# Optimization experiments

Measured on AMD Instinct MI355X. Metric: run time of the kernel, lower is better.

The kernel has to match this reference:

```python
import jax, jax.numpy as jnp
import numpy as np

N = 100_000
E = 1_000_000
F_IN = 128
F_OUT = 64
NHOP = 2


def _xavier(k, shape, gain=1.414):
    fan_in, fan_out = shape
    std = gain * np.sqrt(2.0 / (fan_in + fan_out))
    return (jax.random.normal(k, shape) * std).astype(jnp.float32)


def setup_inputs() -> dict:
    key = jax.random.key(0)
    ks = jax.random.split(key, 8)
    x = jax.random.normal(ks[0], (N, F_IN), jnp.float32)
    edge_index = jax.random.randint(ks[1], (2, E), 0, N)
    edge_attr = jax.random.uniform(ks[2], (E,), jnp.float32)
    W0 = _xavier(ks[3], (F_IN, F_OUT))
    W1 = _xavier(ks[4], (F_IN, F_OUT))
    b0 = jnp.zeros((F_OUT,), jnp.float32)
    b1 = jnp.zeros((F_OUT,), jnp.float32)
    fc0 = _xavier(ks[5], (F_OUT, 1))
    fc1 = _xavier(ks[6], (F_OUT, 1))
    bf0 = jnp.zeros((1,), jnp.float32)
    bf1 = jnp.zeros((1,), jnp.float32)
    return dict(x=x, edge_index=edge_index, edge_attr=edge_attr,
                W0=W0, b0=b0, W1=W1, b1=b1,
                fc0=fc0, bf0=bf0, fc1=fc1, bf1=bf1)


def _spmm(row, col, val, v, n):
    # (A v)[r] = sum over edges (r -> c) of val * v[c]
    return jax.ops.segment_sum(val[:, None] * v[col], row, num_segments=n)


def _adaptive_enc(y, fc, bf):
    # NodeAdaptiveEncoder (eval mode): relu(y) + sigmoid(y@fc+bf) * min(y, 0)
    g = jax.nn.sigmoid(y @ fc + bf)  # [N, 1]
    return jnp.where(y < 0, 0.0, y) + g * jnp.where(y > 0, 0.0, y)


def reference(x, edge_index, edge_attr, W0, b0, W1, b1, fc0, bf0, fc1, bf1):
    n = x.shape[0]
    row, col = edge_index[0], edge_index[1]
    ones = jnp.ones((n, 1), x.dtype)
    params = [(W0, b0, fc0, bf0), (W1, b1, fc1, bf1)]
    outs = []
    for hop in range(NHOP):
        W, b, fc, bf = params[hop]
        h = x @ W  # [N, F_OUT]
        # identity attention; row_uniform norm of A^(hop+1) factors as
        # (A^(hop+1) h) / (A^(hop+1) 1) -- exact since spspmm sums duplicates.
        agg, deg = h, ones
        for _ in range(hop + 1):
            agg = _spmm(row, col, edge_attr, agg, n)
            deg = _spmm(row, col, edge_attr, deg, n)
        safe_deg = jnp.where(deg > 0, deg, 1.0)
        y = jnp.where(deg > 0, agg / safe_deg, 0.0)  # NaN mask for empty rows
        y = y + b
        outs.append(_adaptive_enc(y, fc, bf))
    return jnp.concatenate(outs, axis=1)  # [N, NHOP * F_OUT]
```

## Files before the change

kernel.cpp:

```cpp
#include <hip/hip_runtime.h>

#define F_IN 128
#define F_ALL 128
#define F_HOP 64

#define RPB_BITS 7
#define RPB 128
#define KB_MAX 1024
#define NBLK_BIN 512
#define ECAP 2048

typedef unsigned int uint;
typedef unsigned short ushort;
typedef __attribute__((ext_vector_type(8))) short short8v;
typedef __attribute__((ext_vector_type(4))) float float4v;

__device__ __forceinline__ uint pack_bf16(float lo, float hi) {
    uint ul = __float_as_uint(lo), uh = __float_as_uint(hi);
    ul += 0x7FFFu + ((ul >> 16) & 1u);
    uh += 0x7FFFu + ((uh >> 16) & 1u);
    return (ul >> 16) | (uh & 0xFFFF0000u);
}
__device__ __forceinline__ float bf_lo(uint h) { return __uint_as_float(h << 16); }
__device__ __forceinline__ float bf_hi(uint h) { return __uint_as_float(h & 0xFFFF0000u); }

__global__ __launch_bounds__(256) void gemm_hist_kernel(
    const float* __restrict__ x, const float* __restrict__ W0,
    const float* __restrict__ W1, uint* __restrict__ H2,
    const int* __restrict__ ei, int* __restrict__ bhist,
    int N, int E, int K, int gemmBlocks) {
    __shared__ ushort Wlds[16384];

    if ((int)blockIdx.x >= gemmBlocks) {
        int* h = (int*)Wlds;
        const int hb = blockIdx.x - gemmBlocks;
        for (int i = threadIdx.x; i < K; i += 256) h[i] = 0;
        __syncthreads();
        const int chunk = (E + NBLK_BIN - 1) / NBLK_BIN;
        const int s = hb * chunk;
        const int e = min(s + chunk, E);
        for (int j = s + threadIdx.x; j < e; j += 256)
            atomicAdd(&h[__builtin_nontemporal_load(ei + j) >> RPB_BITS], 1);
        __syncthreads();
        for (int i = threadIdx.x; i < K; i += 256)
            bhist[hb * KB_MAX + i] = h[i];
        return;
    }

    {
        const int t = threadIdx.x;
        #pragma unroll
        for (int i = 0; i < 8; ++i) {
            const int e    = t + 256 * i;
            const int lane = e & 63;
            const int tile = e >> 6;
            const int kt   = tile >> 3;
            const int nt   = tile & 7;
            const int k0   = kt * 32 + (lane >> 4) * 8;
            const int n    = nt * 16 + (lane & 15);
            const float* src = (n < 64) ? (W0 + n) : (W1 + (n - 64));
            float v[8];
            #pragma unroll
            for (int j = 0; j < 8; ++j) v[j] = src[(size_t)(k0 + j) * F_HOP];
            uint4 o;
            o.x = pack_bf16(v[0], v[1]);
            o.y = pack_bf16(v[2], v[3]);
            o.z = pack_bf16(v[4], v[5]);
            o.w = pack_bf16(v[6], v[7]);
            *((uint4*)Wlds + e) = o;
        }
    }
    __syncthreads();

    const int wv   = threadIdx.x >> 6;
    const int lane = threadIdx.x & 63;
    const int rbase = blockIdx.x * 64 + wv * 16;
    if (rbase >= N) return;

    const int m    = lane & 15;
    const int quad = lane >> 4;
    const float* xrow = x + (size_t)(rbase + m) * F_IN + quad * 8;

    float4v acc[8];
    #pragma unroll
    for (int t = 0; t < 8; ++t) acc[t] = (float4v){0.f, 0.f, 0.f, 0.f};

    #pragma unroll
    for (int kt = 0; kt < 4; ++kt) {
        const float4v xa = __builtin_nontemporal_load((const float4v*)(xrow + kt * 32));
        const float4v xb = __builtin_nontemporal_load((const float4v*)(xrow + kt * 32 + 4));
        union { uint4 u; short8v s; } av;
        av.u.x = pack_bf16(xa[0], xa[1]);
        av.u.y = pack_bf16(xa[2], xa[3]);
        av.u.z = pack_bf16(xb[0], xb[1]);
        av.u.w = pack_bf16(xb[2], xb[3]);
        #pragma unroll
        for (int nt = 0; nt < 8; ++nt) {
            union { uint4 u; short8v s; } bv;
            bv.u = *((const uint4*)Wlds + (kt * 8 + nt) * 64 + lane);
            acc[nt] = __builtin_amdgcn_mfma_f32_16x16x32_bf16(av.s, bv.s, acc[nt], 0, 0, 0);
        }
    }

    #pragma unroll
    for (int t = 0; t < 4; ++t) {
        #pragma unroll
        for (int i = 0; i < 4; ++i) {
            const int r = rbase + quad * 4 + i;
            H2[(size_t)r * F_HOP + t * 16 + m] = pack_bf16(acc[t][i], acc[t + 4][i]);
        }
    }
}

__global__ __launch_bounds__(512) void blockscan_kernel(
    int* __restrict__ bhist, int* __restrict__ btot) {
    __shared__ int wsum[8];
    const int b = blockIdx.x;
    const int t = threadIdx.x;
    const int s = bhist[t * KB_MAX + b];
    int v = s;
    #pragma unroll
    for (int d = 1; d < 64; d <<= 1) {
        int u = __shfl_up(v, (unsigned)d, 64);
        if ((t & 63) >= d) v += u;
    }
    if ((t & 63) == 63) wsum[t >> 6] = v;
    __syncthreads();
    int off = 0;
    #pragma unroll
    for (int i = 0; i < 8; ++i) if (i < (t >> 6)) off += wsum[i];
    bhist[t * KB_MAX + b] = off + v - s;
    if (t == 511) btot[b] = off + v;
}

__global__ __launch_bounds__(256) void bin_kernel(
    const int* __restrict__ ei, const float* __restrict__ ea,
    const int* __restrict__ bloc, const int* __restrict__ btot,
    int* __restrict__ bbase_g, int2* __restrict__ gbuf, int E, int K) {
    __shared__ int bb[KB_MAX];
    __shared__ int cur[KB_MAX];
    __shared__ int wsum[4];
    const int t = threadIdx.x;
    const int i0 = 4 * t;
    const int c0 = (i0     < K) ? btot[i0]     : 0;
    const int c1 = (i0 + 1 < K) ? btot[i0 + 1] : 0;
    const int c2 = (i0 + 2 < K) ? btot[i0 + 2] : 0;
    const int c3 = (i0 + 3 < K) ? btot[i0 + 3] : 0;
    const int s = c0 + c1 + c2 + c3;
    int v = s;
    #pragma unroll
    for (int d = 1; d < 64; d <<= 1) {
        int u = __shfl_up(v, (unsigned)d, 64);
        if ((t & 63) >= d) v += u;
    }
    if ((t & 63) == 63) wsum[t >> 6] = v;
    __syncthreads();
    {
        int off = 0;
        #pragma unroll
        for (int i = 0; i < 4; ++i) if (i < (t >> 6)) off += wsum[i];
        const int excl = off + v - s;
        if (i0     < K) bb[i0]     = excl;
        if (i0 + 1 < K) bb[i0 + 1] = excl + c0;
        if (i0 + 2 < K) bb[i0 + 2] = excl + c0 + c1;
        if (i0 + 3 < K) bb[i0 + 3] = excl + c0 + c1 + c2;
    }
    __syncthreads();
    if (blockIdx.x == 0) {
        for (int i = t; i < K; i += 256) bbase_g[i] = bb[i];
        if (t == 0) bbase_g[K] = E;
    }
    for (int i = t; i < K; i += 256)
        cur[i] = bb[i] + bloc[blockIdx.x * KB_MAX + i];
    __syncthreads();
    const int chunk = (E + NBLK_BIN - 1) / NBLK_BIN;
    const int s0 = blockIdx.x * chunk;
    const int e0 = min(s0 + chunk, E);
    for (int j = s0 + t; j < e0; j += 256) {
        const int r = __builtin_nontemporal_load(ei + j);
        const int c = __builtin_nontemporal_load(ei + E + j);
        const int vv = __float_as_int(__builtin_nontemporal_load(ea + j));
        const int b = r >> RPB_BITS;
        const int gp = atomicAdd(&cur[b], 1);
        gbuf[gp] = make_int2(c | ((r & (RPB - 1)) << 17), vv);
    }
}

__global__ __launch_bounds__(512) void pass1_kernel(
    const int* __restrict__ bbase, const int2* __restrict__ gbuf,
    const uint* __restrict__ H2,
    const float* __restrict__ b0, const float* __restrict__ fc0,
    const float* __restrict__ bf0,
    float* __restrict__ out, ushort* __restrict__ T16,
    float* __restrict__ dg1, int N) {
    __shared__ int2 ebuf[ECAP];
    __shared__ int cnt[RPB];
    __shared__ int rp[RPB + 1];
    __shared__ int wsum2[2];
    const int t = threadIdx.x;
    const int b = blockIdx.x;
    const int bstart = bbase[b];
    const int m = bbase[b + 1] - bstart;
    const int mc = (m < ECAP) ? m : ECAP;
    const int row0 = b << RPB_BITS;

    if (t < RPB) cnt[t] = 0;
    __syncthreads();
    for (int j = t; j < mc; j += 512) {
        const int2 p = gbuf[bstart + j];
        ebuf[j] = p;
        atomicAdd(&cnt[(p.x >> 17) & (RPB - 1)], 1);
    }
    __syncthreads();
    int sv = 0, vv = 0;
    if (t < RPB) {
        sv = cnt[t];
        vv = sv;
        #pragma unroll
        for (int d = 1; d < 64; d <<= 1) {
            int u = __shfl_up(vv, (unsigned)d, 64);
            if ((t & 63) >= d) vv += u;
        }
        if ((t & 63) == 63) wsum2[t >> 6] = vv;
    }
    __syncthreads();
    if (t < RPB) rp[t] = ((t >= 64) ? wsum2[0] : 0) + vv - sv;
    if (t == 0) rp[RPB] = mc;
    __syncthreads();
    if (t < RPB) cnt[t] = rp[t];
    __syncthreads();
    int2 pr[4]; int pp[4]; bool pvld[4];
    #pragma unroll
    for (int k2 = 0; k2 < 4; ++k2) {
        const int j = t + 512 * k2;
        pvld[k2] = (j < mc);
        if (pvld[k2]) {
            pr[k2] = ebuf[j];
            pp[k2] = atomicAdd(&cnt[(pr[k2].x >> 17) & (RPB - 1)], 1);
        }
    }
    __syncthreads();
    #pragma unroll
    for (int k2 = 0; k2 < 4; ++k2)
        if (pvld[k2]) ebuf[pp[k2]] = pr[k2];
    __syncthreads();

    const int l  = t & 15;
    const int g  = t >> 4;
    const int f0 = l * 4;
    const uint* __restrict__ H2b = H2 + f0;

    for (int k = 0; k < 4; ++k) {
        const int lr = g * 4 + k;
        const int r = row0 + lr;
        if (r >= N) break;
        const int jb = rp[lr], je = rp[lr + 1];

        float s00 = 0.f, s01 = 0.f, s02 = 0.f, s03 = 0.f;
        float s10 = 0.f, s11 = 0.f, s12 = 0.f, s13 = 0.f;
        float d = 0.f;
        int j = jb;
        for (; j + 4 <= je; j += 4) {
            const int2 e0 = ebuf[j], e1 = ebuf[j + 1], e2 = ebuf[j + 2], e3 = ebuf[j + 3];
            const uint4 h0 = *(const uint4*)(H2b + (size_t)(e0.x & 0x1FFFF) * F_HOP);
            const uint4 h1 = *(const uint4*)(H2b + (size_t)(e1.x & 0x1FFFF) * F_HOP);
            const uint4 h2 = *(const uint4*)(H2b + (size_t)(e2.x & 0x1FFFF) * F_HOP);
            const uint4 h3 = *(const uint4*)(H2b + (size_t)(e3.x & 0x1FFFF) * F_HOP);
            const float v0 = __int_as_float(e0.y), v1 = __int_as_float(e1.y);
            const float v2 = __int_as_float(e2.y), v3 = __int_as_float(e3.y);
            d += (v0 + v1) + (v2 + v3);
            s00 = fmaf(v0, bf_lo(h0.x), s00); s10 = fmaf(v0, bf_hi(h0.x), s10);
            s01 = fmaf(v0, bf_lo(h0.y), s01); s11 = fmaf(v0, bf_hi(h0.y), s11);
            s02 = fmaf(v0, bf_lo(h0.z), s02); s12 = fmaf(v0, bf_hi(h0.z), s12);
            s03 = fmaf(v0, bf_lo(h0.w), s03); s13 = fmaf(v0, bf_hi(h0.w), s13);
            s00 = fmaf(v1, bf_lo(h1.x), s00); s10 = fmaf(v1, bf_hi(h1.x), s10);
            s01 = fmaf(v1, bf_lo(h1.y), s01); s11 = fmaf(v1, bf_hi(h1.y), s11);
            s02 = fmaf(v1, bf_lo(h1.z), s02); s12 = fmaf(v1, bf_hi(h1.z), s12);
            s03 = fmaf(v1, bf_lo(h1.w), s03); s13 = fmaf(v1, bf_hi(h1.w), s13);
            s00 = fmaf(v2, bf_lo(h2.x), s00); s10 = fmaf(v2, bf_hi(h2.x), s10);
            s01 = fmaf(v2, bf_lo(h2.y), s01); s11 = fmaf(v2, bf_hi(h2.y), s11);
            s02 = fmaf(v2, bf_lo(h2.z), s02); s12 = fmaf(v2, bf_hi(h2.z), s12);
            s03 = fmaf(v2, bf_lo(h2.w), s03); s13 = fmaf(v2, bf_hi(h2.w), s13);
            s00 = fmaf(v3, bf_lo(h3.x), s00); s10 = fmaf(v3, bf_hi(h3.x), s10);
            s01 = fmaf(v3, bf_lo(h3.y), s01); s11 = fmaf(v3, bf_hi(h3.y), s11);
            s02 = fmaf(v3, bf_lo(h3.z), s02); s12 = fmaf(v3, bf_hi(h3.z), s12);
            s03 = fmaf(v3, bf_lo(h3.w), s03); s13 = fmaf(v3, bf_hi(h3.w), s13);
        }
        for (; j < je; ++j) {
            const int2 e0 = ebuf[j];
            const uint4 h0 = *(const uint4*)(H2b + (size_t)(e0.x & 0x1FFFF) * F_HOP);
            const float v0 = __int_as_float(e0.y);
            d += v0;
            s00 = fmaf(v0, bf_lo(h0.x), s00); s10 = fmaf(v0, bf_hi(h0.x), s10);
            s01 = fmaf(v0, bf_lo(h0.y), s01); s11 = fmaf(v0, bf_hi(h0.y), s11);
            s02 = fmaf(v0, bf_lo(h0.z), s02); s12 = fmaf(v0, bf_hi(h0.z), s12);
            s03 = fmaf(v0, bf_lo(h0.w), s03); s13 = fmaf(v0, bf_hi(h0.w), s13);
        }
        for (int j2 = ECAP; j2 < m; ++j2) {
            const int2 p = gbuf[bstart + j2];
            if (((p.x >> 17) & (RPB - 1)) == lr) {
                const uint4 h0 = *(const uint4*)(H2b + (size_t)(p.x & 0x1FFFF) * F_HOP);
                const float v0 = __int_as_float(p.y);
                d += v0;
                s00 = fmaf(v0, bf_lo(h0.x), s00); s10 = fmaf(v0, bf_hi(h0.x), s10);
                s01 = fmaf(v0, bf_lo(h0.y), s01); s11 = fmaf(v0, bf_hi(h0.y), s11);
                s02 = fmaf(v0, bf_lo(h0.z), s02); s12 = fmaf(v0, bf_hi(h0.z), s12);
                s03 = fmaf(v0, bf_lo(h0.w), s03); s13 = fmaf(v0, bf_hi(h0.w), s13);
            }
        }

        uint2 tw;
        tw.x = pack_bf16(s10, s11);
        tw.y = pack_bf16(s12, s13);
        *(uint2*)(T16 + (size_t)r * F_HOP + f0) = tw;
        if (l == 0) dg1[r] = d;

        const float inv = (d > 0.f) ? 1.f / d : 0.f;
        const float4 bb4 = *(const float4*)(b0 + f0);
        const float4 ff = *(const float4*)(fc0 + f0);
        const float y0 = s00 * inv + bb4.x;
        const float y1 = s01 * inv + bb4.y;
        const float y2 = s02 * inv + bb4.z;
        const float y3 = s03 * inv + bb4.w;
        float tt = y0 * ff.x + y1 * ff.y + y2 * ff.z + y3 * ff.w;
        #pragma unroll
        for (int mm = 1; mm < 16; mm <<= 1) tt += __shfl_xor(tt, mm, 64);
        const float gg = 1.f / (1.f + __expf(-(tt + bf0[0])));
        float4v o;
        o[0] = fmaxf(y0, 0.f) + gg * fminf(y0, 0.f);
        o[1] = fmaxf(y1, 0.f) + gg * fminf(y1, 0.f);
        o[2] = fmaxf(y2, 0.f) + gg * fminf(y2, 0.f);
        o[3] = fmaxf(y3, 0.f) + gg * fminf(y3, 0.f);
        __builtin_nontemporal_store(o, (float4v*)(out + (size_t)r * F_ALL + f0));
    }
}

__global__ __launch_bounds__(512) void pass2_kernel(
    const int* __restrict__ bbase, const int2* __restrict__ gbuf,
    const ushort* __restrict__ T16, const float* __restrict__ dg1,
    const float* __restrict__ b1, const float* __restrict__ fc1,
    const float* __restrict__ bf1,
    float* __restrict__ out, int N) {
    __shared__ int2 ebuf[ECAP];
    __shared__ int cnt[RPB];
    __shared__ int rp[RPB + 1];
    __shared__ int wsum2[2];
    const int t = threadIdx.x;
    const int b = blockIdx.x;
    const int bstart = bbase[b];
    const int m = bbase[b + 1] - bstart;
    const int mc = (m < ECAP) ? m : ECAP;
    const int row0 = b << RPB_BITS;

    if (t < RPB) cnt[t] = 0;
    __syncthreads();
    for (int j = t; j < mc; j += 512) {
        const int2 p = gbuf[bstart + j];
        ebuf[j] = p;
        atomicAdd(&cnt[(p.x >> 17) & (RPB - 1)], 1);
    }
    __syncthreads();
    int sv = 0, vv = 0;
    if (t < RPB) {
        sv = cnt[t];
        vv = sv;
        #pragma unroll
        for (int d = 1; d < 64; d <<= 1) {
            int u = __shfl_up(vv, (unsigned)d, 64);
            if ((t & 63) >= d) vv += u;
        }
        if ((t & 63) == 63) wsum2[t >> 6] = vv;
    }
    __syncthreads();
    if (t < RPB) rp[t] = ((t >= 64) ? wsum2[0] : 0) + vv - sv;
    if (t == 0) rp[RPB] = mc;
    __syncthreads();
    if (t < RPB) cnt[t] = rp[t];
    __syncthreads();
    int2 pr[4]; int pp[4]; bool pvld[4];
    #pragma unroll
    for (int k2 = 0; k2 < 4; ++k2) {
        const int j = t + 512 * k2;
        pvld[k2] = (j < mc);
        if (pvld[k2]) {
            pr[k2] = ebuf[j];
            pp[k2] = atomicAdd(&cnt[(pr[k2].x >> 17) & (RPB - 1)], 1);
        }
    }
    __syncthreads();
    #pragma unroll
    for (int k2 = 0; k2 < 4; ++k2)
        if (pvld[k2]) ebuf[pp[k2]] = pr[k2];
    __syncthreads();

    const int l  = t & 15;
    const int g  = t >> 4;
    const int f0 = l * 4;
    const ushort* __restrict__ Tb = T16 + f0;

    for (int k = 0; k < 4; ++k) {
        const int lr = g * 4 + k;
        const int r = row0 + lr;
        if (r >= N) break;
        const int jb = rp[lr], je = rp[lr + 1];

        float s0 = 0.f, s1 = 0.f, s2 = 0.f, s3 = 0.f;
        float d2 = 0.f;
        int j = jb;
        for (; j + 4 <= je; j += 4) {
            const int2 e0 = ebuf[j], e1 = ebuf[j + 1], e2 = ebuf[j + 2], e3 = ebuf[j + 3];
            const int c0i = e0.x & 0x1FFFF, c1i = e1.x & 0x1FFFF;
            const int c2i = e2.x & 0x1FFFF, c3i = e3.x & 0x1FFFF;
            const uint2 t0 = *(const uint2*)(Tb + (size_t)c0i * F_HOP);
            const uint2 t1 = *(const uint2*)(Tb + (size_t)c1i * F_HOP);
            const uint2 t2 = *(const uint2*)(Tb + (size_t)c2i * F_HOP);
            const uint2 t3 = *(const uint2*)(Tb + (size_t)c3i * F_HOP);
            const float g0 = dg1[c0i], g1 = dg1[c1i], g2 = dg1[c2i], g3 = dg1[c3i];
            const float v0 = __int_as_float(e0.y), v1 = __int_as_float(e1.y);
            const float v2 = __int_as_float(e2.y), v3 = __int_as_float(e3.y);
            d2 = fmaf(v0, g0, d2); d2 = fmaf(v1, g1, d2);
            d2 = fmaf(v2, g2, d2); d2 = fmaf(v3, g3, d2);
            s0 = fmaf(v0, bf_lo(t0.x), s0); s1 = fmaf(v0, bf_hi(t0.x), s1);
            s2 = fmaf(v0, bf_lo(t0.y), s2); s3 = fmaf(v0, bf_hi(t0.y), s3);
            s0 = fmaf(v1, bf_lo(t1.x), s0); s1 = fmaf(v1, bf_hi(t1.x), s1);
            s2 = fmaf(v1, bf_lo(t1.y), s2); s3 = fmaf(v1, bf_hi(t1.y), s3);
            s0 = fmaf(v2, bf_lo(t2.x), s0); s1 = fmaf(v2, bf_hi(t2.x), s1);
            s2 = fmaf(v2, bf_lo(t2.y), s2); s3 = fmaf(v2, bf_hi(t2.y), s3);
            s0 = fmaf(v3, bf_lo(t3.x), s0); s1 = fmaf(v3, bf_hi(t3.x), s1);
            s2 = fmaf(v3, bf_lo(t3.y), s2); s3 = fmaf(v3, bf_hi(t3.y), s3);
        }
        for (; j < je; ++j) {
            const int2 e0 = ebuf[j];
            const int c0i = e0.x & 0x1FFFF;
            const uint2 t0 = *(const uint2*)(Tb + (size_t)c0i * F_HOP);
            const float v0 = __int_as_float(e0.y);
            d2 = fmaf(v0, dg1[c0i], d2);
            s0 = fmaf(v0, bf_lo(t0.x), s0); s1 = fmaf(v0, bf_hi(t0.x), s1);
            s2 = fmaf(v0, bf_lo(t0.y), s2); s3 = fmaf(v0, bf_hi(t0.y), s3);
        }
        for (int j2 = ECAP; j2 < m; ++j2) {
            const int2 p = gbuf[bstart + j2];
            if (((p.x >> 17) & (RPB - 1)) == lr) {
                const int c0i = p.x & 0x1FFFF;
                const uint2 t0 = *(const uint2*)(Tb + (size_t)c0i * F_HOP);
                const float v0 = __int_as_float(p.y);
                d2 = fmaf(v0, dg1[c0i], d2);
                s0 = fmaf(v0, bf_lo(t0.x), s0); s1 = fmaf(v0, bf_hi(t0.x), s1);
                s2 = fmaf(v0, bf_lo(t0.y), s2); s3 = fmaf(v0, bf_hi(t0.y), s3);
            }
        }

        const float inv = (d2 > 0.f) ? 1.f / d2 : 0.f;
        const float4 bb4 = *(const float4*)(b1 + f0);
        const float4 ff = *(const float4*)(fc1 + f0);
        const float y0 = s0 * inv + bb4.x;
        const float y1 = s1 * inv + bb4.y;
        const float y2 = s2 * inv + bb4.z;
        const float y3 = s3 * inv + bb4.w;
        float tt = y0 * ff.x + y1 * ff.y + y2 * ff.z + y3 * ff.w;
        #pragma unroll
        for (int mm = 1; mm < 16; mm <<= 1) tt += __shfl_xor(tt, mm, 64);
        const float gg = 1.f / (1.f + __expf(-(tt + bf1[0])));
        float4v o;
        o[0] = fmaxf(y0, 0.f) + gg * fminf(y0, 0.f);
        o[1] = fmaxf(y1, 0.f) + gg * fminf(y1, 0.f);
        o[2] = fmaxf(y2, 0.f) + gg * fminf(y2, 0.f);
        o[3] = fmaxf(y3, 0.f) + gg * fminf(y3, 0.f);
        __builtin_nontemporal_store(o, (float4v*)(out + (size_t)r * F_ALL + F_HOP + f0));
    }
}

extern "C" void kernel_launch(void* const* d_in, const int* in_sizes, int n_in,
                              void* d_out, int out_size, void* d_ws, size_t ws_size,
                              hipStream_t stream) {
    const float* x   = (const float*)d_in[0];
    const int*   ei  = (const int*)  d_in[1];
    const float* ea  = (const float*)d_in[2];
    const float* W0  = (const float*)d_in[3];
    const float* b0  = (const float*)d_in[4];
    const float* W1  = (const float*)d_in[5];
    const float* b1  = (const float*)d_in[6];
    const float* fc0 = (const float*)d_in[7];
    const float* bf0 = (const float*)d_in[8];
    const float* fc1 = (const float*)d_in[9];
    const float* bf1 = (const float*)d_in[10];
    float* out = (float*)d_out;

    const int N = in_sizes[0] / F_IN;
    const int E = in_sizes[2];
    const int K = (N + RPB - 1) >> RPB_BITS;

    uint*   H2   = (uint*)d_ws;
    ushort* T16  = (ushort*)(H2 + (size_t)N * F_HOP);
    float*  dg1  = (float*)(T16 + (size_t)N * F_HOP);
    int2*   gbuf = (int2*)(dg1 + (size_t)((N + 3) & ~3));
    int*    bhist = (int*)(gbuf + (size_t)E);
    int*    btot  = bhist + (size_t)NBLK_BIN * KB_MAX;
    int*    bbase = btot + (KB_MAX + 4);

    const int gemmBlocks = (N + 63) / 64;
    gemm_hist_kernel<<<gemmBlocks + NBLK_BIN, 256, 0, stream>>>(
        x, W0, W1, H2, ei, bhist, N, E, K, gemmBlocks);

    blockscan_kernel<<<K, 512, 0, stream>>>(bhist, btot);
    bin_kernel<<<NBLK_BIN, 256, 0, stream>>>(ei, ea, bhist, btot, bbase, gbuf, E, K);

    pass1_kernel<<<K, 512, 0, stream>>>(
        bbase, gbuf, H2, b0, fc0, bf0, out, T16, dg1, N);

    pass2_kernel<<<K, 512, 0, stream>>>(
        bbase, gbuf, T16, dg1, b1, fc1, bf1, out, N);
}
```

Measured before the change: 240.5 us.

## Replace scan-based edge binning with fixed-capacity buckets built in the GEMM kernel

Drops the two-level histogram scan and the separate bin kernel. Each build block now reserves a slice of a fixed-capacity per-bucket buffer with global atomics and scatters its edges directly, all inside the GEMM launch. Buckets shrink to 64 rows with 256-thread aggregation blocks. Edges beyond the capacity go to a global overflow list that every overflowing block scans linearly. This removes two kernel launches and a global scan, at the cost of a memset, global atomic contention, padded storage, and possibly slow overflow handling on skewed graphs.

```diff
diff --git a/kernel.cpp b/kernel.cpp
--- a/kernel.cpp
+++ b/kernel.cpp
@@ -4,11 +4,12 @@
 #define F_ALL 128
 #define F_HOP 64
 
-#define RPB_BITS 7
-#define RPB 128
-#define KB_MAX 1024
-#define NBLK_BIN 512
-#define ECAP 2048
+#define RPB_BITS 6
+#define RPB 64
+#define KB_MAX 2048
+#define NBLK_BUILD 256
+#define CAP 1024
+#define OVF_CAP 65536
 
 typedef unsigned int uint;
 typedef unsigned short ushort;
@@ -24,31 +25,51 @@
 __device__ __forceinline__ float bf_lo(uint h) { return __uint_as_float(h << 16); }
 __device__ __forceinline__ float bf_hi(uint h) { return __uint_as_float(h & 0xFFFF0000u); }
 
-__global__ __launch_bounds__(256) void gemm_hist_kernel(
+__global__ __launch_bounds__(256) void gemm_build_kernel(
     const float* __restrict__ x, const float* __restrict__ W0,
     const float* __restrict__ W1, uint* __restrict__ H2,
-    const int* __restrict__ ei, int* __restrict__ bhist,
-    int N, int E, int K, int gemmBlocks) {
+    const int* __restrict__ ei, const float* __restrict__ ea,
+    int* __restrict__ gcnt,
+    int* __restrict__ ovfCnt, int4* __restrict__ ovf,
+    int2* __restrict__ gbuf, int N, int E, int K) {
     __shared__ ushort Wlds[16384];
 
-    if ((int)blockIdx.x >= gemmBlocks) {
-        int* h = (int*)Wlds;
-        const int hb = blockIdx.x - gemmBlocks;
-        for (int i = threadIdx.x; i < K; i += 256) h[i] = 0;
+    const int t = threadIdx.x;
+    if ((int)blockIdx.x < NBLK_BUILD) {
+        int* h   = (int*)Wlds;
+        int* cur = h + KB_MAX;
+        const int hb = blockIdx.x;
+        for (int i = t; i < K; i += 256) h[i] = 0;
         __syncthreads();
-        const int chunk = (E + NBLK_BIN - 1) / NBLK_BIN;
+        const int chunk = (E + NBLK_BUILD - 1) / NBLK_BUILD;
         const int s = hb * chunk;
         const int e = min(s + chunk, E);
-        for (int j = s + threadIdx.x; j < e; j += 256)
+        for (int j = s + t; j < e; j += 256)
             atomicAdd(&h[__builtin_nontemporal_load(ei + j) >> RPB_BITS], 1);
         __syncthreads();
-        for (int i = threadIdx.x; i < K; i += 256)
-            bhist[hb * KB_MAX + i] = h[i];
+        for (int b = t; b < K; b += 256) {
+            const int hc = h[b];
+            if (hc) cur[b] = atomicAdd(&gcnt[b * 16], hc);
+        }
+        __syncthreads();
+        for (int j = s + t; j < e; j += 256) {
+            const int r = ei[j];
+            const int c = ei[E + j];
+            const int vv = __float_as_int(ea[j]);
+            const int b = r >> RPB_BITS;
+            const int w0 = c | ((r & (RPB - 1)) << 17);
+            const int pos = atomicAdd(&cur[b], 1);
+            if (pos < CAP) {
+                gbuf[(size_t)b * CAP + pos] = make_int2(w0, vv);
+            } else {
+                const int op = atomicAdd(ovfCnt, 1);
+                if (op < OVF_CAP) ovf[op] = make_int4(b, w0, vv, 0);
+            }
+        }
         return;
     }
 
     {
-        const int t = threadIdx.x;
         #pragma unroll
         for (int i = 0; i < 8; ++i) {
             const int e    = t + 256 * i;
@@ -72,9 +93,9 @@
     }
     __syncthreads();
 
-    const int wv   = threadIdx.x >> 6;
-    const int lane = threadIdx.x & 63;
-    const int rbase = blockIdx.x * 64 + wv * 16;
+    const int wv   = t >> 6;
+    const int lane = t & 63;
+    const int rbase = (blockIdx.x - NBLK_BUILD) * 64 + wv * 16;
     if (rbase >= N) return;
 
     const int m    = lane & 15;
@@ -83,7 +104,7 @@
 
     float4v acc[8];
     #pragma unroll
-    for (int t = 0; t < 8; ++t) acc[t] = (float4v){0.f, 0.f, 0.f, 0.f};
+    for (int tt = 0; tt < 8; ++tt) acc[tt] = (float4v){0.f, 0.f, 0.f, 0.f};
 
     #pragma unroll
     for (int kt = 0; kt < 4; ++kt) {
@@ -103,136 +124,60 @@
     }
 
     #pragma unroll
-    for (int t = 0; t < 4; ++t) {
+    for (int tt = 0; tt < 4; ++tt) {
         #pragma unroll
         for (int i = 0; i < 4; ++i) {
             const int r = rbase + quad * 4 + i;
-            H2[(size_t)r * F_HOP + t * 16 + m] = pack_bf16(acc[t][i], acc[t + 4][i]);
+            H2[(size_t)r * F_HOP + tt * 16 + m] = pack_bf16(acc[tt][i], acc[tt + 4][i]);
         }
     }
 }
 
-__global__ __launch_bounds__(512) void blockscan_kernel(
-    int* __restrict__ bhist, int* __restrict__ btot) {
-    __shared__ int wsum[8];
-    const int b = blockIdx.x;
-    const int t = threadIdx.x;
-    const int s = bhist[t * KB_MAX + b];
-    int v = s;
-    #pragma unroll
-    for (int d = 1; d < 64; d <<= 1) {
-        int u = __shfl_up(v, (unsigned)d, 64);
-        if ((t & 63) >= d) v += u;
-    }
-    if ((t & 63) == 63) wsum[t >> 6] = v;
-    __syncthreads();
-    int off = 0;
-    #pragma unroll
-    for (int i = 0; i < 8; ++i) if (i < (t >> 6)) off += wsum[i];
-    bhist[t * KB_MAX + b] = off + v - s;
-    if (t == 511) btot[b] = off + v;
-}
-
-__global__ __launch_bounds__(256) void bin_kernel(
-    const int* __restrict__ ei, const float* __restrict__ ea,
-    const int* __restrict__ bloc, const int* __restrict__ btot,
-    int* __restrict__ bbase_g, int2* __restrict__ gbuf, int E, int K) {
-    __shared__ int bb[KB_MAX];
-    __shared__ int cur[KB_MAX];
-    __shared__ int wsum[4];
-    const int t = threadIdx.x;
-    const int i0 = 4 * t;
-    const int c0 = (i0     < K) ? btot[i0]     : 0;
-    const int c1 = (i0 + 1 < K) ? btot[i0 + 1] : 0;
-    const int c2 = (i0 + 2 < K) ? btot[i0 + 2] : 0;
-    const int c3 = (i0 + 3 < K) ? btot[i0 + 3] : 0;
-    const int s = c0 + c1 + c2 + c3;
-    int v = s;
-    #pragma unroll
-    for (int d = 1; d < 64; d <<= 1) {
-        int u = __shfl_up(v, (unsigned)d, 64);
-        if ((t & 63) >= d) v += u;
-    }
-    if ((t & 63) == 63) wsum[t >> 6] = v;
-    __syncthreads();
-    {
-        int off = 0;
-        #pragma unroll
-        for (int i = 0; i < 4; ++i) if (i < (t >> 6)) off += wsum[i];
-        const int excl = off + v - s;
-        if (i0     < K) bb[i0]     = excl;
-        if (i0 + 1 < K) bb[i0 + 1] = excl + c0;
-        if (i0 + 2 < K) bb[i0 + 2] = excl + c0 + c1;
-        if (i0 + 3 < K) bb[i0 + 3] = excl + c0 + c1 + c2;
-    }
-    __syncthreads();
-    if (blockIdx.x == 0) {
-        for (int i = t; i < K; i += 256) bbase_g[i] = bb[i];
-        if (t == 0) bbase_g[K] = E;
-    }
-    for (int i = t; i < K; i += 256)
-        cur[i] = bb[i] + bloc[blockIdx.x * KB_MAX + i];
-    __syncthreads();
-    const int chunk = (E + NBLK_BIN - 1) / NBLK_BIN;
-    const int s0 = blockIdx.x * chunk;
-    const int e0 = min(s0 + chunk, E);
-    for (int j = s0 + t; j < e0; j += 256) {
-        const int r = __builtin_nontemporal_load(ei + j);
-        const int c = __builtin_nontemporal_load(ei + E + j);
-        const int vv = __float_as_int(__builtin_nontemporal_load(ea + j));
-        const int b = r >> RPB_BITS;
-        const int gp = atomicAdd(&cur[b], 1);
-        gbuf[gp] = make_int2(c | ((r & (RPB - 1)) << 17), vv);
-    }
-}
-
-__global__ __launch_bounds__(512) void pass1_kernel(
-    const int* __restrict__ bbase, const int2* __restrict__ gbuf,
+__global__ __launch_bounds__(256) void pass1_kernel(
+    const int* __restrict__ gcnt, const int2* __restrict__ gbuf,
+    const int* __restrict__ ovfCnt, const int4* __restrict__ ovf,
     const uint* __restrict__ H2,
     const float* __restrict__ b0, const float* __restrict__ fc0,
     const float* __restrict__ bf0,
     float* __restrict__ out, ushort* __restrict__ T16,
     float* __restrict__ dg1, int N) {
-    __shared__ int2 ebuf[ECAP];
+    __shared__ int2 ebuf[CAP];
     __shared__ int cnt[RPB];
     __shared__ int rp[RPB + 1];
-    __shared__ int wsum2[2];
     const int t = threadIdx.x;
     const int b = blockIdx.x;
-    const int bstart = bbase[b];
-    const int m = bbase[b + 1] - bstart;
-    const int mc = (m < ECAP) ? m : ECAP;
+    const int cntb = gcnt[b * 16];
+    const int mc = (cntb < CAP) ? cntb : CAP;
+    const int ovfn = (cntb > CAP) ? min(*ovfCnt, OVF_CAP) : 0;
     const int row0 = b << RPB_BITS;
+    const int2* __restrict__ gb = gbuf + (size_t)b * CAP;
 
     if (t < RPB) cnt[t] = 0;
     __syncthreads();
-    for (int j = t; j < mc; j += 512) {
-        const int2 p = gbuf[bstart + j];
+    for (int j = t; j < mc; j += 256) {
+        const int2 p = gb[j];
         ebuf[j] = p;
         atomicAdd(&cnt[(p.x >> 17) & (RPB - 1)], 1);
     }
     __syncthreads();
-    int sv = 0, vv = 0;
     if (t < RPB) {
-        sv = cnt[t];
-        vv = sv;
+        const int sv = cnt[t];
+        int vv = sv;
         #pragma unroll
         for (int d = 1; d < 64; d <<= 1) {
             int u = __shfl_up(vv, (unsigned)d, 64);
-            if ((t & 63) >= d) vv += u;
-        }
-        if ((t & 63) == 63) wsum2[t >> 6] = vv;
-    }
-    __syncthreads();
-    if (t < RPB) rp[t] = ((t >= 64) ? wsum2[0] : 0) + vv - sv;
-    if (t == 0) rp[RPB] = mc;
+            if (t >= d) vv += u;
+        }
+        rp[t] = vv - sv;
+        if (t == RPB - 1) rp[RPB] = mc;
+    }
     __syncthreads();
     if (t < RPB) cnt[t] = rp[t];
     __syncthreads();
     int2 pr[4]; int pp[4]; bool pvld[4];
     #pragma unroll
     for (int k2 = 0; k2 < 4; ++k2) {
-        const int j = t + 512 * k2;
+        const int j = t + 256 * k2;
         pvld[k2] = (j < mc);
         if (pvld[k2]) {
             pr[k2] = ebuf[j];
@@ -296,11 +241,11 @@
             s02 = fmaf(v0, bf_lo(h0.z), s02); s12 = fmaf(v0, bf_hi(h0.z), s12);
             s03 = fmaf(v0, bf_lo(h0.w), s03); s13 = fmaf(v0, bf_hi(h0.w), s13);
         }
-        for (int j2 = ECAP; j2 < m; ++j2) {
-            const int2 p = gbuf[bstart + j2];
-            if (((p.x >> 17) & (RPB - 1)) == lr) {
-                const uint4 h0 = *(const uint4*)(H2b + (size_t)(p.x & 0x1FFFF) * F_HOP);
-                const float v0 = __int_as_float(p.y);
+        for (int j2 = 0; j2 < ovfn; ++j2) {
+            const int4 p = ovf[j2];
+            if (p.x == b && (((p.y >> 17) & (RPB - 1)) == lr)) {
+                const uint4 h0 = *(const uint4*)(H2b + (size_t)(p.y & 0x1FFFF) * F_HOP);
+                const float v0 = __int_as_float(p.z);
                 d += v0;
                 s00 = fmaf(v0, bf_lo(h0.x), s00); s10 = fmaf(v0, bf_hi(h0.x), s10);
                 s01 = fmaf(v0, bf_lo(h0.y), s01); s11 = fmaf(v0, bf_hi(h0.y), s11);
@@ -335,52 +280,50 @@
     }
 }
 
-__global__ __launch_bounds__(512) void pass2_kernel(
-    const int* __restrict__ bbase, const int2* __restrict__ gbuf,
+__global__ __launch_bounds__(256) void pass2_kernel(
+    const int* __restrict__ gcnt, const int2* __restrict__ gbuf,
+    const int* __restrict__ ovfCnt, const int4* __restrict__ ovf,
     const ushort* __restrict__ T16, const float* __restrict__ dg1,
     const float* __restrict__ b1, const float* __restrict__ fc1,
     const float* __restrict__ bf1,
     float* __restrict__ out, int N) {
-    __shared__ int2 ebuf[ECAP];
+    __shared__ int2 ebuf[CAP];
     __shared__ int cnt[RPB];
     __shared__ int rp[RPB + 1];
-    __shared__ int wsum2[2];
     const int t = threadIdx.x;
     const int b = blockIdx.x;
-    const int bstart = bbase[b];
-    const int m = bbase[b + 1] - bstart;
-    const int mc = (m < ECAP) ? m : ECAP;
+    const int cntb = gcnt[b * 16];
+    const int mc = (cntb < CAP) ? cntb : CAP;
+    const int ovfn = (cntb > CAP) ? min(*ovfCnt, OVF_CAP) : 0;
     const int row0 = b << RPB_BITS;
+    const int2* __restrict__ gb = gbuf + (size_t)b * CAP;
 
     if (t < RPB) cnt[t] = 0;
     __syncthreads();
-    for (int j = t; j < mc; j += 512) {
-        const int2 p = gbuf[bstart + j];
+    for (int j = t; j < mc; j += 256) {
+        const int2 p = gb[j];
         ebuf[j] = p;
         atomicAdd(&cnt[(p.x >> 17) & (RPB - 1)], 1);
     }
     __syncthreads();
-    int sv = 0, vv = 0;
     if (t < RPB) {
-        sv = cnt[t];
-        vv = sv;
+        const int sv = cnt[t];
+        int vv = sv;
         #pragma unroll
         for (int d = 1; d < 64; d <<= 1) {
             int u = __shfl_up(vv, (unsigned)d, 64);
-            if ((t & 63) >= d) vv += u;
-        }
-        if ((t & 63) == 63) wsum2[t >> 6] = vv;
-    }
-    __syncthreads();
-    if (t < RPB) rp[t] = ((t >= 64) ? wsum2[0] : 0) + vv - sv;
-    if (t == 0) rp[RPB] = mc;
+            if (t >= d) vv += u;
+        }
+        rp[t] = vv - sv;
+        if (t == RPB - 1) rp[RPB] = mc;
+    }
     __syncthreads();
     if (t < RPB) cnt[t] = rp[t];
     __syncthreads();
     int2 pr[4]; int pp[4]; bool pvld[4];
     #pragma unroll
     for (int k2 = 0; k2 < 4; ++k2) {
-        const int j = t + 512 * k2;
+        const int j = t + 256 * k2;
         pvld[k2] = (j < mc);
         if (pvld[k2]) {
             pr[k2] = ebuf[j];
@@ -438,12 +381,12 @@
             s0 = fmaf(v0, bf_lo(t0.x), s0); s1 = fmaf(v0, bf_hi(t0.x), s1);
             s2 = fmaf(v0, bf_lo(t0.y), s2); s3 = fmaf(v0, bf_hi(t0.y), s3);
         }
-        for (int j2 = ECAP; j2 < m; ++j2) {
-            const int2 p = gbuf[bstart + j2];
-            if (((p.x >> 17) & (RPB - 1)) == lr) {
-                const int c0i = p.x & 0x1FFFF;
+        for (int j2 = 0; j2 < ovfn; ++j2) {
+            const int4 p = ovf[j2];
+            if (p.x == b && (((p.y >> 17) & (RPB - 1)) == lr)) {
+                const int c0i = p.y & 0x1FFFF;
                 const uint2 t0 = *(const uint2*)(Tb + (size_t)c0i * F_HOP);
-                const float v0 = __int_as_float(p.y);
+                const float v0 = __int_as_float(p.z);
                 d2 = fmaf(v0, dg1[c0i], d2);
                 s0 = fmaf(v0, bf_lo(t0.x), s0); s1 = fmaf(v0, bf_hi(t0.x), s1);
                 s2 = fmaf(v0, bf_lo(t0.y), s2); s3 = fmaf(v0, bf_hi(t0.y), s3);
@@ -493,21 +436,20 @@
     uint*   H2   = (uint*)d_ws;
     ushort* T16  = (ushort*)(H2 + (size_t)N * F_HOP);
     float*  dg1  = (float*)(T16 + (size_t)N * F_HOP);
-    int2*   gbuf = (int2*)(dg1 + (size_t)((N + 3) & ~3));
-    int*    bhist = (int*)(gbuf + (size_t)E);
-    int*    btot  = bhist + (size_t)NBLK_BIN * KB_MAX;
-    int*    bbase = btot + (KB_MAX + 4);
+    int*    gcnt = (int*)(dg1 + (size_t)((N + 3) & ~3));
+    int*    ovfCnt = gcnt + (size_t)K * 16;
+    int2*   gbuf = (int2*)(ovfCnt + 16);
+    int4*   ovf  = (int4*)(gbuf + (size_t)K * CAP);
+
+    hipMemsetAsync(gcnt, 0, ((size_t)K * 16 + 16) * sizeof(int), stream);
 
     const int gemmBlocks = (N + 63) / 64;
-    gemm_hist_kernel<<<gemmBlocks + NBLK_BIN, 256, 0, stream>>>(
-        x, W0, W1, H2, ei, bhist, N, E, K, gemmBlocks);
-
-    blockscan_kernel<<<K, 512, 0, stream>>>(bhist, btot);
-    bin_kernel<<<NBLK_BIN, 256, 0, stream>>>(ei, ea, bhist, btot, bbase, gbuf, E, K);
-
-    pass1_kernel<<<K, 512, 0, stream>>>(
-        bbase, gbuf, H2, b0, fc0, bf0, out, T16, dg1, N);
-
-    pass2_kernel<<<K, 512, 0, stream>>>(
-        bbase, gbuf, T16, dg1, b1, fc1, bf1, out, N);
+    gemm_build_kernel<<<NBLK_BUILD + gemmBlocks, 256, 0, stream>>>(
+        x, W0, W1, H2, ei, ea, gcnt, ovfCnt, ovf, gbuf, N, E, K);
+
+    pass1_kernel<<<K, 256, 0, stream>>>(
+        gcnt, gbuf, ovfCnt, ovf, H2, b0, fc0, bf0, out, T16, dg1, N);
+
+    pass2_kernel<<<K, 256, 0, stream>>>(
+        gcnt, gbuf, ovfCnt, ovf, T16, dg1, b1, fc1, bf1, out, N);
 }
```

Result: faster. 234.2 us (-2.6%).
